# Kernel optimization log

Hardware: AMD Instinct MI355X
Metric: run time of the kernel (lower is better)

The kernel has to match this reference:

```python
import jax, jax.numpy as jnp
import numpy as np

# Fixed genome topology (layered DAG, topologically ordered levels)
B = 4096      # batch
N_IN = 512    # input nodes
H1 = 1536     # hidden level 1
H2 = 1536     # hidden level 2
N_OUT = 512   # output nodes
FAN = 32      # fan-in per non-input node


def setup_inputs() -> dict:
    key = jax.random.key(0)
    ks = jax.random.split(key, 10)
    x = jax.random.normal(ks[0], (B, N_IN), dtype=jnp.float32)
    # level 1: sources among inputs [0, N_IN)
    src0 = jax.random.randint(ks[1], (H1 * FAN,), 0, N_IN, dtype=jnp.int32)
    dst0 = jax.random.randint(ks[2], (H1 * FAN,), 0, H1, dtype=jnp.int32)
    w0 = jax.random.normal(ks[3], (H1 * FAN,), dtype=jnp.float32) * 0.1
    # level 2: sources among inputs + level1 [0, N_IN+H1)
    src1 = jax.random.randint(ks[4], (H2 * FAN,), 0, N_IN + H1, dtype=jnp.int32)
    dst1 = jax.random.randint(ks[5], (H2 * FAN,), 0, H2, dtype=jnp.int32)
    w1 = jax.random.normal(ks[6], (H2 * FAN,), dtype=jnp.float32) * 0.1
    # output level: sources among all earlier nodes [0, N_IN+H1+H2)
    src2 = jax.random.randint(ks[7], (N_OUT * FAN,), 0, N_IN + H1 + H2, dtype=jnp.int32)
    dst2 = jax.random.randint(ks[8], (N_OUT * FAN,), 0, N_OUT, dtype=jnp.int32)
    w2 = jax.random.normal(ks[9], (N_OUT * FAN,), dtype=jnp.float32) * 0.1
    return dict(x=x, src0=src0, dst0=dst0, w0=w0,
                src1=src1, dst1=dst1, w1=w1,
                src2=src2, dst2=dst2, w2=w2)


def _level(node_values, src, dst, w, size):
    # per-edge weighted gather: [B, E]
    vals = node_values[:, src] * w
    # scatter-add into destination nodes of this level: [B, size]
    agg = jnp.zeros((node_values.shape[0], size), node_values.dtype).at[:, dst].add(vals)
    # per-node activation (genome.activation == 'relu'); relu(0)=0 matches
    # original's behavior of leaving unconnected nodes at zero
    return jax.nn.relu(agg)


def reference(x, src0, dst0, w0, src1, dst1, w1, src2, dst2, w2):
    nv = x                                        # [B, N_IN]
    h1 = _level(nv, src0, dst0, w0, H1)           # [B, H1]
    nv = jnp.concatenate([nv, h1], axis=1)        # [B, N_IN+H1]
    h2 = _level(nv, src1, dst1, w1, H2)           # [B, H2]
    nv = jnp.concatenate([nv, h2], axis=1)        # [B, N_IN+H1+H2]
    out = _level(nv, src2, dst2, w2, N_OUT)       # [B, N_OUT]
    return out
```

## Files before the change

### kernel.cpp

```cpp
#include <hip/hip_runtime.h>
#include <hip/hip_fp16.h>
#include <stdint.h>

#define BATCH 4096
#define N_IN  512
#define H1    1536
#define H2    1536
#define N_OUT 512
#define FAN   32
#define E0 (H1 * FAN)
#define E1 (H2 * FAN)
#define E2 (N_OUT * FAN)
#define K1 N_IN
#define K2 (N_IN + H1)
#define K3 (N_IN + H1 + H2)

#define NVSTRIDE 3584
#define NVBYTES  ((size_t)BATCH * NVSTRIDE * 2)
#define W0BYTES  ((size_t)H1 * K1 * 2)
#define W1BYTES  ((size_t)H2 * K2 * 2)
#define W2BYTES  ((size_t)N_OUT * K3 * 2)

typedef _Float16 f16x8 __attribute__((ext_vector_type(8)));
typedef float    f32x4 __attribute__((ext_vector_type(4)));

#define GLL(SRC, DST)                                                        \
    __builtin_amdgcn_global_load_lds(                                        \
        (const __attribute__((address_space(1))) void*)(const void*)(SRC),   \
        (__attribute__((address_space(3))) void*)(void*)(DST), 16, 0, 0)

__global__ __launch_bounds__(256) void k_xcvt(const float* __restrict__ x,
                                              __half* __restrict__ nvT) {
    const int t  = blockIdx.x * 256 + threadIdx.x;
    const int n  = t >> 6;
    const int c8 = t & 63;
    const float4 f0 = *(const float4*)(x + (size_t)n * N_IN + c8 * 8);
    const float4 f1 = *(const float4*)(x + (size_t)n * N_IN + c8 * 8 + 4);
    const __half2 a = __floats2half2_rn(f0.x, f0.y);
    const __half2 b = __floats2half2_rn(f0.z, f0.w);
    const __half2 c = __floats2half2_rn(f1.x, f1.y);
    const __half2 d = __floats2half2_rn(f1.z, f1.w);
    uint4 u;
    u.x = *(const uint32_t*)&a; u.y = *(const uint32_t*)&b;
    u.z = *(const uint32_t*)&c; u.w = *(const uint32_t*)&d;
    *(uint4*)(nvT + (size_t)n * NVSTRIDE + c8 * 8) = u;
}

__device__ __forceinline__ void atomic_add_half(__half* addr, float val) {
    uint32_t* base = (uint32_t*)((size_t)addr & ~(size_t)3);
    const bool hi  = ((size_t)addr & 2) != 0;
    uint32_t old = *base, assumed;
    do {
        assumed = old;
        __half2 h2 = *(__half2*)&assumed;
        float f = (hi ? __high2float(h2) : __low2float(h2)) + val;
        __half2 nh = hi ? __halves2half2(__low2half(h2), __float2half_rn(f))
                        : __halves2half2(__float2half_rn(f), __high2half(h2));
        old = atomicCAS(base, assumed, *(uint32_t*)&nh);
    } while (old != assumed);
}

__global__ __launch_bounds__(256) void k_wfill01(
        const int* __restrict__ s0, const int* __restrict__ d0, const float* __restrict__ w0,
        const int* __restrict__ s1, const int* __restrict__ d1, const float* __restrict__ w1,
        __half* __restrict__ W0d, __half* __restrict__ W1d) {
    const int e = blockIdx.x * 256 + threadIdx.x;
    if (e < E0)  atomic_add_half(W0d + (size_t)d0[e] * K1 + s0[e], w0[e]);
    else { const int i = e - E0; atomic_add_half(W1d + (size_t)d1[i] * K2 + s1[i], w1[i]); }
}

__global__ __launch_bounds__(256) void k_wfill(const int* __restrict__ src,
                                               const int* __restrict__ dst,
                                               const float* __restrict__ w,
                                               __half* __restrict__ Wd, const int K) {
    const int e = blockIdx.x * 256 + threadIdx.x;
    atomic_add_half(Wd + (size_t)dst[e] * K + src[e], w[e]);
}

__global__ __launch_bounds__(256, 2)
void k_gemm96(const __half* __restrict__ A,
              const __half* __restrict__ Bt,
              __half* __restrict__ Ch,
              const int K) {
    __shared__ __half lA[2][96 * 64];
    __shared__ __half lB[2][128 * 64];
    const int tid  = threadIdx.x;
    const int lane = tid & 63;
    const int wv   = tid >> 6;
    const int wr   = wv >> 1, wc = wv & 1;
    const int m0   = blockIdx.y * 96;
    const int n0   = blockIdx.x * 128;
    const int lrow = lane >> 3;
    const int lchk = lane & 7;

    f32x4 acc[3][4] = {};

#define STAGE96(BUF, KT) {                                                   \
    _Pragma("unroll")                                                        \
    for (int it = 0; it < 3; ++it) {                                         \
        const int row = it * 32 + wv * 8 + lrow;                             \
        const int sc  = lchk ^ (row & 7);                                    \
        GLL(A + (size_t)(m0 + row) * K + (KT) + sc * 8,                      \
            lA[BUF] + (it * 32 + wv * 8) * 64);                              \
    }                                                                        \
    _Pragma("unroll")                                                        \
    for (int it = 0; it < 4; ++it) {                                         \
        const int row = it * 32 + wv * 8 + lrow;                             \
        const int sc  = lchk ^ (row & 7);                                    \
        GLL(Bt + (size_t)(n0 + row) * NVSTRIDE + (KT) + sc * 8,              \
            lB[BUF] + (it * 32 + wv * 8) * 64);                              \
    }                                                                        \
}

    const int NT = K >> 6;
    STAGE96(0, 0)
    int cur = 0;
    for (int t = 0; t < NT; ++t) {
        __builtin_amdgcn_s_barrier();
        __builtin_amdgcn_sched_barrier(0);
        if (t + 1 < NT) {
            STAGE96(cur ^ 1, (t + 1) << 6)
            asm volatile("s_waitcnt vmcnt(7)" ::: "memory");
        } else {
            asm volatile("s_waitcnt vmcnt(0)" ::: "memory");
        }
        __builtin_amdgcn_sched_barrier(0);
        __builtin_amdgcn_s_barrier();
        __builtin_amdgcn_sched_barrier(0);
#pragma unroll
        for (int kk = 0; kk < 2; ++kk) {
            f16x8 af[3], bf[4];
#pragma unroll
            for (int fm = 0; fm < 3; ++fm) {
                const int row = wr * 48 + fm * 16 + (lane & 15);
                const int ch  = (kk * 4 + (lane >> 4)) ^ (row & 7);
                af[fm] = *(const f16x8*)(lA[cur] + row * 64 + ch * 8);
            }
#pragma unroll
            for (int fn = 0; fn < 4; ++fn) {
                const int row = wc * 64 + fn * 16 + (lane & 15);
                const int ch  = (kk * 4 + (lane >> 4)) ^ (row & 7);
                bf[fn] = *(const f16x8*)(lB[cur] + row * 64 + ch * 8);
            }
#pragma unroll
            for (int fm = 0; fm < 3; ++fm)
#pragma unroll
                for (int fn = 0; fn < 4; ++fn)
                    acc[fm][fn] = __builtin_amdgcn_mfma_f32_16x16x32_f16(
                        af[fm], bf[fn], acc[fm][fn], 0, 0, 0);
        }
        cur ^= 1;
    }
#undef STAGE96

    const int cm = (lane >> 4) << 2;
    const int cn = lane & 15;
#pragma unroll
    for (int fm = 0; fm < 3; ++fm)
#pragma unroll
        for (int fn = 0; fn < 4; ++fn) {
            const f32x4 v = acc[fm][fn];
            const __half2 p0 = __floats2half2_rn(fmaxf(v[0], 0.f), fmaxf(v[1], 0.f));
            const __half2 p1 = __floats2half2_rn(fmaxf(v[2], 0.f), fmaxf(v[3], 0.f));
            const int mm = m0 + wr * 48 + fm * 16 + cm;
            const int nn = n0 + wc * 64 + fn * 16 + cn;
            uint2 u; u.x = *(const uint32_t*)&p0; u.y = *(const uint32_t*)&p1;
            *(uint2*)(Ch + (size_t)nn * NVSTRIDE + mm) = u;
        }
}

__global__ __launch_bounds__(512, 2)
void k_gemm3(const __half* __restrict__ A,
             const __half* __restrict__ Bt,
             float* __restrict__ Cf) {
    __shared__ __half lA[4][64 * 64];
    __shared__ __half lB[4][128 * 64];
    const int tid  = threadIdx.x;
    const int lane = tid & 63;
    const int wv   = tid >> 6;
    const int wr   = wv >> 2, wc = wv & 3;
    const int m0   = blockIdx.y * 64;
    const int n0   = blockIdx.x * 128;
    const int lrow = lane >> 3;
    const int lchk = lane & 7;
    const int K = K3;

    f32x4 acc[2][2] = {};

#define STAGE3(BUF, KT) {                                                    \
    _Pragma("unroll")                                                        \
    for (int i = 0; i < 3; ++i) {                                            \
        const int L = wv * 3 + i;                   \
        if (L < 8) {                                                         \
            const int row = L * 8 + lrow;                                    \
            const int sc  = lchk ^ (row & 7);                                \
            GLL(A + (size_t)(m0 + row) * K + (KT) + sc * 8,                  \
                lA[BUF] + L * 512);                                          \
        } else {                                                             \
            const int row = (L - 8) * 8 + lrow;                              \
            const int sc  = lchk ^ (row & 7);                                \
            GLL(Bt + (size_t)(n0 + row) * NVSTRIDE + (KT) + sc * 8,          \
                lB[BUF] + (L - 8) * 512);                                    \
        }                                                                    \
    }                                                                        \
}

    const int NT = K >> 6;
    STAGE3(0, 0)
    STAGE3(1, 64)
    for (int t = 0; t < NT; ++t) {
        if (t + 2 < NT) {
            STAGE3((t + 2) & 3, (t + 2) << 6)
            asm volatile("s_waitcnt vmcnt(6)" ::: "memory");
        } else if (t + 1 < NT) {
            asm volatile("s_waitcnt vmcnt(3)" ::: "memory");
        } else {
            asm volatile("s_waitcnt vmcnt(0)" ::: "memory");
        }
        __builtin_amdgcn_sched_barrier(0);
        __builtin_amdgcn_s_barrier();
        __builtin_amdgcn_sched_barrier(0);
        const __half* bA = lA[t & 3];
        const __half* bB = lB[t & 3];
#pragma unroll
        for (int kk = 0; kk < 2; ++kk) {
            f16x8 af[2], bf[2];
#pragma unroll
            for (int fm = 0; fm < 2; ++fm) {
                const int row = wr * 32 + fm * 16 + (lane & 15);
                const int ch  = (kk * 4 + (lane >> 4)) ^ (row & 7);
                af[fm] = *(const f16x8*)(bA + row * 64 + ch * 8);
            }
#pragma unroll
            for (int fn = 0; fn < 2; ++fn) {
                const int row = wc * 32 + fn * 16 + (lane & 15);
                const int ch  = (kk * 4 + (lane >> 4)) ^ (row & 7);
                bf[fn] = *(const f16x8*)(bB + row * 64 + ch * 8);
            }
#pragma unroll
            for (int fm = 0; fm < 2; ++fm)
#pragma unroll
                for (int fn = 0; fn < 2; ++fn)
                    acc[fm][fn] = __builtin_amdgcn_mfma_f32_16x16x32_f16(
                        af[fm], bf[fn], acc[fm][fn], 0, 0, 0);
        }
    }
#undef STAGE3

    const int cm = (lane >> 4) << 2;
    const int cn = lane & 15;
#pragma unroll
    for (int fm = 0; fm < 2; ++fm)
#pragma unroll
        for (int fn = 0; fn < 2; ++fn) {
            const f32x4 v = acc[fm][fn];
            float4 o;
            o.x = fmaxf(v[0], 0.f); o.y = fmaxf(v[1], 0.f);
            o.z = fmaxf(v[2], 0.f); o.w = fmaxf(v[3], 0.f);
            const int mm = m0 + wr * 32 + fm * 16 + cm;
            const int nn = n0 + wc * 32 + fn * 16 + cn;
            *(float4*)(Cf + (size_t)nn * N_OUT + mm) = o;
        }
}

extern "C" void kernel_launch(void* const* d_in, const int* in_sizes, int n_in,
                              void* d_out, int out_size, void* d_ws, size_t ws_size,
                              hipStream_t stream) {
    const float* x  = (const float*)d_in[0];
    const int* s0   = (const int*)d_in[1];
    const int* dd0  = (const int*)d_in[2];
    const float* w0 = (const float*)d_in[3];
    const int* s1   = (const int*)d_in[4];
    const int* dd1  = (const int*)d_in[5];
    const float* w1 = (const float*)d_in[6];
    const int* s2   = (const int*)d_in[7];
    const int* dd2  = (const int*)d_in[8];
    const float* w2 = (const float*)d_in[9];

    char*   ws  = (char*)d_ws;
    __half* nvT = (__half*)ws;
    __half* W0p = (__half*)(ws + NVBYTES);
    __half* W1p = (__half*)(ws + NVBYTES + W0BYTES);
    __half* W2p = W0p;
    float*  out = (float*)d_out;

    k_xcvt<<<BATCH * 64 / 256, 256, 0, stream>>>(x, nvT);

    hipMemsetAsync(W0p, 0, W0BYTES + W1BYTES, stream);
    k_wfill01<<<(E0 + E1) / 256, 256, 0, stream>>>(s0, dd0, w0, s1, dd1, w1, W0p, W1p);
    k_gemm96<<<dim3(BATCH / 128, H1 / 96), 256, 0, stream>>>(W0p, nvT, nvT + N_IN, K1);
    k_gemm96<<<dim3(BATCH / 128, H2 / 96), 256, 0, stream>>>(W1p, nvT, nvT + K2, K2);

    hipMemsetAsync(W2p, 0, W2BYTES, stream);
    k_wfill<<<E2 / 256, 256, 0, stream>>>(s2, dd2, w2, W2p, K3);
    k_gemm3<<<dim3(BATCH / 128, N_OUT / 64), 512, 0, stream>>>(W2p, nvT, out);
}
```

Baseline: 161.4 us.

## Deepen gemm96 pipeline to 4 LDS stages with 8 warps and fuse memset

The level-1/2 GEMM kernel moves from 4 to 8 waves per block, splits global-to-LDS loading between A-loading and B-loading waves, and uses a 4-buffer ring with prefetch distance 2 and one barrier per k-step instead of two. The memset of the dense weight matrices is folded into the input conversion kernel so one launch does both. This aims to hide load latency better and cut launch and sync overhead. In exchange it uses twice the LDS per block, which can lower occupancy, and each wave does less MFMA work per LDS fragment load.

```diff
diff --git a/kernel.cpp b/kernel.cpp
--- a/kernel.cpp
+++ b/kernel.cpp
@@ -20,6 +20,7 @@
 #define W0BYTES  ((size_t)H1 * K1 * 2)
 #define W1BYTES  ((size_t)H2 * K2 * 2)
 #define W2BYTES  ((size_t)N_OUT * K3 * 2)
+#define WZU4  ((W0BYTES + W1BYTES) / 16)
 
 typedef _Float16 f16x8 __attribute__((ext_vector_type(8)));
 typedef float    f32x4 __attribute__((ext_vector_type(4)));
@@ -29,21 +30,28 @@
         (const __attribute__((address_space(1))) void*)(const void*)(SRC),   \
         (__attribute__((address_space(3))) void*)(void*)(DST), 16, 0, 0)
 
-__global__ __launch_bounds__(256) void k_xcvt(const float* __restrict__ x,
-                                              __half* __restrict__ nvT) {
-    const int t  = blockIdx.x * 256 + threadIdx.x;
-    const int n  = t >> 6;
-    const int c8 = t & 63;
-    const float4 f0 = *(const float4*)(x + (size_t)n * N_IN + c8 * 8);
-    const float4 f1 = *(const float4*)(x + (size_t)n * N_IN + c8 * 8 + 4);
-    const __half2 a = __floats2half2_rn(f0.x, f0.y);
-    const __half2 b = __floats2half2_rn(f0.z, f0.w);
-    const __half2 c = __floats2half2_rn(f1.x, f1.y);
-    const __half2 d = __floats2half2_rn(f1.z, f1.w);
-    uint4 u;
-    u.x = *(const uint32_t*)&a; u.y = *(const uint32_t*)&b;
-    u.z = *(const uint32_t*)&c; u.w = *(const uint32_t*)&d;
-    *(uint4*)(nvT + (size_t)n * NVSTRIDE + c8 * 8) = u;
+__global__ __launch_bounds__(256) void k_xcvt_zero(const float* __restrict__ x,
+                                                   __half* __restrict__ nvT,
+                                                   uint4* __restrict__ Wz) {
+    const int b = blockIdx.x;
+    if (b < 1024) {
+        const int t  = b * 256 + threadIdx.x;
+        const int n  = t >> 6;
+        const int c8 = t & 63;
+        const float4 f0 = *(const float4*)(x + (size_t)n * N_IN + c8 * 8);
+        const float4 f1 = *(const float4*)(x + (size_t)n * N_IN + c8 * 8 + 4);
+        const __half2 a = __floats2half2_rn(f0.x, f0.y);
+        const __half2 bb = __floats2half2_rn(f0.z, f0.w);
+        const __half2 c = __floats2half2_rn(f1.x, f1.y);
+        const __half2 d = __floats2half2_rn(f1.z, f1.w);
+        uint4 u;
+        u.x = *(const uint32_t*)&a; u.y = *(const uint32_t*)&bb;
+        u.z = *(const uint32_t*)&c; u.w = *(const uint32_t*)&d;
+        *(uint4*)(nvT + (size_t)n * NVSTRIDE + c8 * 8) = u;
+    } else {
+        const int i = (b - 1024) * 256 + threadIdx.x;
+        if (i < WZU4) Wz[i] = make_uint4(0, 0, 0, 0);
+    }
 }
 
 __device__ __forceinline__ void atomic_add_half(__half* addr, float val) {
@@ -77,93 +85,101 @@
     atomic_add_half(Wd + (size_t)dst[e] * K + src[e], w[e]);
 }
 
-__global__ __launch_bounds__(256, 2)
+__global__ __launch_bounds__(512, 2)
 void k_gemm96(const __half* __restrict__ A,
               const __half* __restrict__ Bt,
               __half* __restrict__ Ch,
               const int K) {
-    __shared__ __half lA[2][96 * 64];
-    __shared__ __half lB[2][128 * 64];
+    __shared__ __half lA[4][96 * 64];
+    __shared__ __half lB[4][128 * 64];
     const int tid  = threadIdx.x;
     const int lane = tid & 63;
     const int wv   = tid >> 6;
-    const int wr   = wv >> 1, wc = wv & 1;
+    const int wr   = wv >> 2, wc = wv & 3;
     const int m0   = blockIdx.y * 96;
     const int n0   = blockIdx.x * 128;
     const int lrow = lane >> 3;
     const int lchk = lane & 7;
 
-    f32x4 acc[3][4] = {};
-
-#define STAGE96(BUF, KT) {                                                   \
-    _Pragma("unroll")                                                        \
-    for (int it = 0; it < 3; ++it) {                                         \
-        const int row = it * 32 + wv * 8 + lrow;                             \
-        const int sc  = lchk ^ (row & 7);                                    \
-        GLL(A + (size_t)(m0 + row) * K + (KT) + sc * 8,                      \
-            lA[BUF] + (it * 32 + wv * 8) * 64);                              \
+    f32x4 acc[3][2] = {};
+
+#define STG96(BUF, KT) {                                                     \
+    if (wv < 4) {                                                            \
+        _Pragma("unroll")                                                    \
+        for (int i = 0; i < 3; ++i) {                                        \
+            const int g   = wv * 3 + i;           \
+            const int row = g * 8 + lrow;                                    \
+            const int sc  = lchk ^ (row & 7);                                \
+            GLL(A + (size_t)(m0 + row) * K + (KT) + sc * 8,                  \
+                lA[BUF] + g * 512);                                          \
+        }                                                                    \
+    } else {                                                                 \
+        _Pragma("unroll")                                                    \
+        for (int i = 0; i < 4; ++i) {                                        \
+            const int g   = (wv - 4) * 4 + i;     \
+            const int row = g * 8 + lrow;                                    \
+            const int sc  = lchk ^ (row & 7);                                \
+            GLL(Bt + (size_t)(n0 + row) * NVSTRIDE + (KT) + sc * 8,          \
+                lB[BUF] + g * 512);                                          \
+        }                                                                    \
     }                                                                        \
-    _Pragma("unroll")                                                        \
-    for (int it = 0; it < 4; ++it) {                                         \
-        const int row = it * 32 + wv * 8 + lrow;                             \
-        const int sc  = lchk ^ (row & 7);                                    \
-        GLL(Bt + (size_t)(n0 + row) * NVSTRIDE + (KT) + sc * 8,              \
-            lB[BUF] + (it * 32 + wv * 8) * 64);                              \
-    }                                                                        \
 }
 
     const int NT = K >> 6;
-    STAGE96(0, 0)
-    int cur = 0;
+    STG96(0, 0)
+    STG96(1, 64)
     for (int t = 0; t < NT; ++t) {
-        __builtin_amdgcn_s_barrier();
-        __builtin_amdgcn_sched_barrier(0);
-        if (t + 1 < NT) {
-            STAGE96(cur ^ 1, (t + 1) << 6)
-            asm volatile("s_waitcnt vmcnt(7)" ::: "memory");
+        if (t + 2 < NT) {
+            STG96((t + 2) & 3, (t + 2) << 6)
+            if (wv < 4) asm volatile("s_waitcnt vmcnt(6)" ::: "memory");
+            else        asm volatile("s_waitcnt vmcnt(8)" ::: "memory");
+        } else if (t + 1 < NT) {
+            if (wv < 4) asm volatile("s_waitcnt vmcnt(3)" ::: "memory");
+            else        asm volatile("s_waitcnt vmcnt(4)" ::: "memory");
         } else {
             asm volatile("s_waitcnt vmcnt(0)" ::: "memory");
         }
         __builtin_amdgcn_sched_barrier(0);
         __builtin_amdgcn_s_barrier();
         __builtin_amdgcn_sched_barrier(0);
+        const __half* bA = lA[t & 3];
+        const __half* bB = lB[t & 3];
 #pragma unroll
         for (int kk = 0; kk < 2; ++kk) {
-            f16x8 af[3], bf[4];
+            f16x8 af[3], bf[2];
 #pragma unroll
             for (int fm = 0; fm < 3; ++fm) {
                 const int row = wr * 48 + fm * 16 + (lane & 15);
                 const int ch  = (kk * 4 + (lane >> 4)) ^ (row & 7);
-                af[fm] = *(const f16x8*)(lA[cur] + row * 64 + ch * 8);
+                af[fm] = *(const f16x8*)(bA + row * 64 + ch * 8);
             }
 #pragma unroll
-            for (int fn = 0; fn < 4; ++fn) {
-                const int row = wc * 64 + fn * 16 + (lane & 15);
+            for (int fn = 0; fn < 2; ++fn) {
+                const int row = wc * 32 + fn * 16 + (lane & 15);
                 const int ch  = (kk * 4 + (lane >> 4)) ^ (row & 7);
-                bf[fn] = *(const f16x8*)(lB[cur] + row * 64 + ch * 8);
+                bf[fn] = *(const f16x8*)(bB + row * 64 + ch * 8);
             }
 #pragma unroll
             for (int fm = 0; fm < 3; ++fm)
 #pragma unroll
-                for (int fn = 0; fn < 4; ++fn)
+                for (int fn = 0; fn < 2; ++fn)
                     acc[fm][fn] = __builtin_amdgcn_mfma_f32_16x16x32_f16(
                         af[fm], bf[fn], acc[fm][fn], 0, 0, 0);
         }
-        cur ^= 1;
     }
-#undef STAGE96
+#undef STG96
 
     const int cm = (lane >> 4) << 2;
     const int cn = lane & 15;
 #pragma unroll
     for (int fm = 0; fm < 3; ++fm)
 #pragma unroll
-        for (int fn = 0; fn < 4; ++fn) {
+        for (int fn = 0; fn < 2; ++fn) {
             const f32x4 v = acc[fm][fn];
             const __half2 p0 = __floats2half2_rn(fmaxf(v[0], 0.f), fmaxf(v[1], 0.f));
             const __half2 p1 = __floats2half2_rn(fmaxf(v[2], 0.f), fmaxf(v[3], 0.f));
             const int mm = m0 + wr * 48 + fm * 16 + cm;
-            const int nn = n0 + wc * 64 + fn * 16 + cn;
+            const int nn = n0 + wc * 32 + fn * 16 + cn;
             uint2 u; u.x = *(const uint32_t*)&p0; u.y = *(const uint32_t*)&p1;
             *(uint2*)(Ch + (size_t)nn * NVSTRIDE + mm) = u;
         }
@@ -284,12 +300,11 @@
     __half* W2p = W0p;
     float*  out = (float*)d_out;
 
-    k_xcvt<<<BATCH * 64 / 256, 256, 0, stream>>>(x, nvT);
-
-    hipMemsetAsync(W0p, 0, W0BYTES + W1BYTES, stream);
+    k_xcvt_zero<<<1024 + (WZU4 + 255) / 256, 256, 0, stream>>>(x, nvT, (uint4*)W0p);
+
     k_wfill01<<<(E0 + E1) / 256, 256, 0, stream>>>(s0, dd0, w0, s1, dd1, w1, W0p, W1p);
-    k_gemm96<<<dim3(BATCH / 128, H1 / 96), 256, 0, stream>>>(W0p, nvT, nvT + N_IN, K1);
-    k_gemm96<<<dim3(BATCH / 128, H2 / 96), 256, 0, stream>>>(W1p, nvT, nvT + K2, K2);
+    k_gemm96<<<dim3(BATCH / 128, H1 / 96), 512, 0, stream>>>(W0p, nvT, nvT + N_IN, K1);
+    k_gemm96<<<dim3(BATCH / 128, H2 / 96), 512, 0, stream>>>(W1p, nvT, nvT + K2, K2);
 
     hipMemsetAsync(W2p, 0, W2BYTES, stream);
     k_wfill<<<E2 / 256, 256, 0, stream>>>(s2, dd2, w2, W2p, K3);
```

After: 167.7 us. 1.04x slower.

## Fuse weight zeroing into input conversion, merge all weight fills, deepen gemm3 pipeline

Applied to the files above, without the earlier changes.

Zeroing of the dense weight buffers moves into the input-conversion kernel, replacing the separate memset calls. When the workspace is large enough, all three levels' sparse-to-dense weight scatters run in one kernel, with W2 in its own buffer. The final GEMM goes from a 4-slot to a 5-slot LDS ring with prefetch distance 3, to hide more global-load latency. This cuts launch count and serialization, but the extra LDS (~120KB per block) may lower occupancy for the final GEMM.

```diff
diff --git a/kernel.cpp b/kernel.cpp
--- a/kernel.cpp
+++ b/kernel.cpp
@@ -11,6 +11,7 @@
 #define E0 (H1 * FAN)
 #define E1 (H2 * FAN)
 #define E2 (N_OUT * FAN)
+#define ETOT (E0 + E1 + E2)
 #define K1 N_IN
 #define K2 (N_IN + H1)
 #define K3 (N_IN + H1 + H2)
@@ -20,6 +21,8 @@
 #define W0BYTES  ((size_t)H1 * K1 * 2)
 #define W1BYTES  ((size_t)H2 * K2 * 2)
 #define W2BYTES  ((size_t)N_OUT * K3 * 2)
+#define WZ01U4   ((W0BYTES + W1BYTES) / 16)
+#define WZALLU4  ((W0BYTES + W1BYTES + W2BYTES) / 16)
 
 typedef _Float16 f16x8 __attribute__((ext_vector_type(8)));
 typedef float    f32x4 __attribute__((ext_vector_type(4)));
@@ -29,21 +32,29 @@
         (const __attribute__((address_space(1))) void*)(const void*)(SRC),   \
         (__attribute__((address_space(3))) void*)(void*)(DST), 16, 0, 0)
 
-__global__ __launch_bounds__(256) void k_xcvt(const float* __restrict__ x,
-                                              __half* __restrict__ nvT) {
-    const int t  = blockIdx.x * 256 + threadIdx.x;
-    const int n  = t >> 6;
-    const int c8 = t & 63;
-    const float4 f0 = *(const float4*)(x + (size_t)n * N_IN + c8 * 8);
-    const float4 f1 = *(const float4*)(x + (size_t)n * N_IN + c8 * 8 + 4);
-    const __half2 a = __floats2half2_rn(f0.x, f0.y);
-    const __half2 b = __floats2half2_rn(f0.z, f0.w);
-    const __half2 c = __floats2half2_rn(f1.x, f1.y);
-    const __half2 d = __floats2half2_rn(f1.z, f1.w);
-    uint4 u;
-    u.x = *(const uint32_t*)&a; u.y = *(const uint32_t*)&b;
-    u.z = *(const uint32_t*)&c; u.w = *(const uint32_t*)&d;
-    *(uint4*)(nvT + (size_t)n * NVSTRIDE + c8 * 8) = u;
+__global__ __launch_bounds__(256) void k_xcvt_zero(const float* __restrict__ x,
+                                                   __half* __restrict__ nvT,
+                                                   uint4* __restrict__ Wz,
+                                                   const int nzu4) {
+    const int b = blockIdx.x;
+    if (b < 1024) {
+        const int t  = b * 256 + threadIdx.x;
+        const int n  = t >> 6;
+        const int c8 = t & 63;
+        const float4 f0 = *(const float4*)(x + (size_t)n * N_IN + c8 * 8);
+        const float4 f1 = *(const float4*)(x + (size_t)n * N_IN + c8 * 8 + 4);
+        const __half2 a = __floats2half2_rn(f0.x, f0.y);
+        const __half2 bb = __floats2half2_rn(f0.z, f0.w);
+        const __half2 c = __floats2half2_rn(f1.x, f1.y);
+        const __half2 d = __floats2half2_rn(f1.z, f1.w);
+        uint4 u;
+        u.x = *(const uint32_t*)&a; u.y = *(const uint32_t*)&bb;
+        u.z = *(const uint32_t*)&c; u.w = *(const uint32_t*)&d;
+        *(uint4*)(nvT + (size_t)n * NVSTRIDE + c8 * 8) = u;
+    } else {
+        const int i = (b - 1024) * 256 + threadIdx.x;
+        if (i < nzu4) Wz[i] = make_uint4(0, 0, 0, 0);
+    }
 }
 
 __device__ __forceinline__ void atomic_add_half(__half* addr, float val) {
@@ -58,6 +69,17 @@
                         : __halves2half2(__float2half_rn(f), __high2half(h2));
         old = atomicCAS(base, assumed, *(uint32_t*)&nh);
     } while (old != assumed);
+}
+
+__global__ __launch_bounds__(256) void k_wfill_all(
+        const int* __restrict__ s0, const int* __restrict__ d0, const float* __restrict__ w0,
+        const int* __restrict__ s1, const int* __restrict__ d1, const float* __restrict__ w1,
+        const int* __restrict__ s2, const int* __restrict__ d2, const float* __restrict__ w2,
+        __half* __restrict__ W0d, __half* __restrict__ W1d, __half* __restrict__ W2d) {
+    const int e = blockIdx.x * 256 + threadIdx.x;
+    if (e < E0)            atomic_add_half(W0d + (size_t)d0[e] * K1 + s0[e], w0[e]);
+    else if (e < E0 + E1) { const int i = e - E0;      atomic_add_half(W1d + (size_t)d1[i] * K2 + s1[i], w1[i]); }
+    else                  { const int i = e - E0 - E1; atomic_add_half(W2d + (size_t)d2[i] * K3 + s2[i], w2[i]); }
 }
 
 __global__ __launch_bounds__(256) void k_wfill01(
@@ -173,8 +195,8 @@
 void k_gemm3(const __half* __restrict__ A,
              const __half* __restrict__ Bt,
              float* __restrict__ Cf) {
-    __shared__ __half lA[4][64 * 64];
-    __shared__ __half lB[4][128 * 64];
+    __shared__ __half lA[5][64 * 64];
+    __shared__ __half lB[5][128 * 64];
     const int tid  = threadIdx.x;
     const int lane = tid & 63;
     const int wv   = tid >> 6;
@@ -208,9 +230,14 @@
     const int NT = K >> 6;
     STAGE3(0, 0)
     STAGE3(1, 64)
+    STAGE3(2, 128)
+    int sc_ = 0;
+    int sp3 = 3;
     for (int t = 0; t < NT; ++t) {
-        if (t + 2 < NT) {
-            STAGE3((t + 2) & 3, (t + 2) << 6)
+        if (t + 3 < NT) {
+            STAGE3(sp3, (t + 3) << 6)
+            asm volatile("s_waitcnt vmcnt(9)" ::: "memory");
+        } else if (t + 2 < NT) {
             asm volatile("s_waitcnt vmcnt(6)" ::: "memory");
         } else if (t + 1 < NT) {
             asm volatile("s_waitcnt vmcnt(3)" ::: "memory");
@@ -220,8 +247,8 @@
         __builtin_amdgcn_sched_barrier(0);
         __builtin_amdgcn_s_barrier();
         __builtin_amdgcn_sched_barrier(0);
-        const __half* bA = lA[t & 3];
-        const __half* bB = lB[t & 3];
+        const __half* bA = lA[sc_];
+        const __half* bB = lB[sc_];
 #pragma unroll
         for (int kk = 0; kk < 2; ++kk) {
             f16x8 af[2], bf[2];
@@ -244,6 +271,8 @@
                     acc[fm][fn] = __builtin_amdgcn_mfma_f32_16x16x32_f16(
                         af[fm], bf[fn], acc[fm][fn], 0, 0, 0);
         }
+        sc_ = (sc_ == 4) ? 0 : sc_ + 1;
+        sp3 = (sp3 == 4) ? 0 : sp3 + 1;
     }
 #undef STAGE3
 
@@ -281,17 +310,26 @@
     __half* nvT = (__half*)ws;
     __half* W0p = (__half*)(ws + NVBYTES);
     __half* W1p = (__half*)(ws + NVBYTES + W0BYTES);
-    __half* W2p = W0p;
     float*  out = (float*)d_out;
 
-    k_xcvt<<<BATCH * 64 / 256, 256, 0, stream>>>(x, nvT);
-
-    hipMemsetAsync(W0p, 0, W0BYTES + W1BYTES, stream);
-    k_wfill01<<<(E0 + E1) / 256, 256, 0, stream>>>(s0, dd0, w0, s1, dd1, w1, W0p, W1p);
-    k_gemm96<<<dim3(BATCH / 128, H1 / 96), 256, 0, stream>>>(W0p, nvT, nvT + N_IN, K1);
-    k_gemm96<<<dim3(BATCH / 128, H2 / 96), 256, 0, stream>>>(W1p, nvT, nvT + K2, K2);
-
-    hipMemsetAsync(W2p, 0, W2BYTES, stream);
-    k_wfill<<<E2 / 256, 256, 0, stream>>>(s2, dd2, w2, W2p, K3);
-    k_gemm3<<<dim3(BATCH / 128, N_OUT / 64), 512, 0, stream>>>(W2p, nvT, out);
-}
+    if (ws_size >= NVBYTES + W0BYTES + W1BYTES + W2BYTES) {
+        __half* W2p = (__half*)(ws + NVBYTES + W0BYTES + W1BYTES);
+        k_xcvt_zero<<<1024 + (WZALLU4 + 255) / 256, 256, 0, stream>>>(
+            x, nvT, (uint4*)W0p, (int)WZALLU4);
+        k_wfill_all<<<ETOT / 256, 256, 0, stream>>>(s0, dd0, w0, s1, dd1, w1,
+                                                    s2, dd2, w2, W0p, W1p, W2p);
+        k_gemm96<<<dim3(BATCH / 128, H1 / 96), 256, 0, stream>>>(W0p, nvT, nvT + N_IN, K1);
+        k_gemm96<<<dim3(BATCH / 128, H2 / 96), 256, 0, stream>>>(W1p, nvT, nvT + K2, K2);
+        k_gemm3<<<dim3(BATCH / 128, N_OUT / 64), 512, 0, stream>>>(W2p, nvT, out);
+    } else {
+        __half* W2p = W0p;
+        k_xcvt_zero<<<1024 + (WZ01U4 + 255) / 256, 256, 0, stream>>>(
+            x, nvT, (uint4*)W0p, (int)WZ01U4);
+        k_wfill01<<<(E0 + E1) / 256, 256, 0, stream>>>(s0, dd0, w0, s1, dd1, w1, W0p, W1p);
+        k_gemm96<<<dim3(BATCH / 128, H1 / 96), 256, 0, stream>>>(W0p, nvT, nvT + N_IN, K1);
+        k_gemm96<<<dim3(BATCH / 128, H2 / 96), 256, 0, stream>>>(W1p, nvT, nvT + K2, K2);
+        hipMemsetAsync(W2p, 0, W2BYTES, stream);
+        k_wfill<<<E2 / 256, 256, 0, stream>>>(s2, dd2, w2, W2p, K3);
+        k_gemm3<<<dim3(BATCH / 128, N_OUT / 64), 512, 0, stream>>>(W2p, nvT, out);
+    }
+}
```

Measured after the change: 156.9 us. 2.7% less time.
